# Kernel optimization log

Measured on AMD Instinct MI355X. Metric: run time of the kernel, lower is better.

Reference implementation:

```python
import jax, jax.numpy as jnp
import numpy as np

B, D, L, H = 8, 512, 2048, 8
DH = D // H
NEG = -1e30


def setup_inputs() -> dict:
    key = jax.random.key(0)
    k1, k2, k3, k4 = jax.random.split(key, 4)
    queries = jax.random.normal(k1, (B, D, L), dtype=jnp.float32)
    mask = jax.random.randint(k2, (B, L), 0, 2, dtype=jnp.int32)
    w_mem = jax.random.normal(k3, (2 * D, D), dtype=jnp.float32) * (1.0 / np.sqrt(D))
    w_q = jax.random.normal(k4, (D, D), dtype=jnp.float32) * (1.0 / np.sqrt(D))
    return {"queries": queries, "mask": mask, "w_mem": w_mem, "w_q": w_q}


def reference(queries, mask, w_mem, w_q):
    # 1x1 conv == pointwise GEMM over channel dim. queries: [B, D, L]
    memory = jnp.einsum('od,bdl->blo', w_mem, queries)  # [B, L, 2D]
    query = jnp.einsum('od,bdl->blo', w_q, queries)     # [B, L, D]

    def split_heads(x):  # [B, L, C] -> [B, H, L, C/H]
        b, l, c = x.shape
        return x.reshape(b, l, H, c // H).transpose(0, 2, 1, 3)

    k, v = memory[..., :D], memory[..., D:]
    Q = split_heads(query) * (DH ** -0.5)  # [B, H, L, DH]
    K = split_heads(k)
    V = split_heads(v)

    logits = jnp.einsum('bhqd,bhkd->bhqk', Q, K)  # [B, H, L, L]
    m = mask.astype(jnp.float32)[:, None, None, :]  # [B, 1, 1, L]
    logits = logits * m + (1.0 - m) * NEG
    weights = jax.nn.softmax(logits, axis=-1)
    x = jnp.einsum('bhqk,bhkd->bhqd', weights, V)  # [B, H, L, DH]
    # combine heads -> [B, L, D] -> transpose back to [B, D, L]
    out = x.transpose(0, 2, 1, 3).reshape(B, L, D).transpose(0, 2, 1)
    return out
```

## Files before the change

### kernel.cpp

```cpp
#include <hip/hip_runtime.h>
#include <hip/hip_bf16.h>

#define NB 8
#define ND 512
#define NL 2048
#define NH 8
#define NDH 64
#define VROWS 72

typedef __attribute__((ext_vector_type(8))) short bf16x8;
typedef __attribute__((ext_vector_type(4))) float f32x4;
typedef __attribute__((ext_vector_type(4))) unsigned int u32x4;

__device__ __forceinline__ unsigned short f2bf(float x) {
    return (unsigned short)((__float_as_uint(x) + 0x8000u) >> 16);
}

__device__ __forceinline__ float exp2_fast(float x) {
#if __has_builtin(__builtin_amdgcn_exp2f)
    return __builtin_amdgcn_exp2f(x);
#else
    return exp2f(x);
#endif
}

__device__ __forceinline__ unsigned int pack_bf16(float a, float b) {
#if __has_builtin(__builtin_amdgcn_cvt_pk_bf16_f32)
    auto r = __builtin_amdgcn_cvt_pk_bf16_f32(a, b);
    unsigned int u;
    __builtin_memcpy(&u, &r, 4);
    return u;
#else
    unsigned int ua = __float_as_uint(a) + 0x8000u;
    unsigned int ub = __float_as_uint(b) + 0x8000u;
    return __builtin_amdgcn_perm(ub, ua, 0x07060302u);
#endif
}

__device__ __forceinline__ void async16(void* lds, const void* g) {
    __builtin_amdgcn_global_load_lds(
        (const __attribute__((address_space(1))) unsigned int*)g,
        (__attribute__((address_space(3))) unsigned int*)lds, 16, 0, 0);
}

__global__ __launch_bounds__(256) void prep(
    const float* __restrict__ qin,
    const float* __restrict__ w_mem, const float* __restrict__ w_q,
    const int* __restrict__ maskp,
    unsigned short* __restrict__ Xt, unsigned short* __restrict__ Wc,
    unsigned short* __restrict__ Vt)
{
    const int bid = blockIdx.x;
    const int t = threadIdx.x;
    if (bid < 2048) {
        __shared__ __align__(16) unsigned short T[64][72];
        const int l0 = (bid & 31) * 64, d0 = ((bid >> 5) & 7) * 64, b = bid >> 8;
        const float* X = qin + ((size_t)b * ND + d0) * NL + l0;
        #pragma unroll
        for (int i = 0; i < 4; ++i) {
            int e = t + i * 256;
            int d = e >> 4, l4 = (e & 15) * 4;
            float4 v = *(const float4*)(X + (size_t)d * NL + l4);
            T[l4 + 0][d] = f2bf(v.x);
            T[l4 + 1][d] = f2bf(v.y);
            T[l4 + 2][d] = f2bf(v.z);
            T[l4 + 3][d] = f2bf(v.w);
        }
        __syncthreads();
        #pragma unroll
        for (int i = 0; i < 2; ++i) {
            int e = t + i * 256;
            int row = e >> 3, c8 = (e & 7) * 8;
            *(bf16x8*)(Xt + ((size_t)b * NL + l0 + row) * ND + d0 + c8) =
                *(const bf16x8*)&T[row][c8];
        }
    } else if (bid < 2432) {
        int idx = ((bid - 2048) * 256 + t) * 8;
        int o = idx >> 9, k = idx & 511;
        const float* src;
        float sc;
        if (o < 1024) { src = w_mem + (size_t)o * ND + k; sc = 1.0f; }
        else          { src = w_q + (size_t)(o - 1024) * ND + k;
                        sc = 0.125f * 1.4426950408889634f; }
        float4 f0 = *(const float4*)src;
        float4 f1 = *(const float4*)(src + 4);
        ushort4 p0 = { f2bf(f0.x * sc), f2bf(f0.y * sc), f2bf(f0.z * sc), f2bf(f0.w * sc) };
        ushort4 p1 = { f2bf(f1.x * sc), f2bf(f1.y * sc), f2bf(f1.z * sc), f2bf(f1.w * sc) };
        *(ushort4*)(Wc + idx) = p0;
        *(ushort4*)(Wc + idx + 4) = p1;
    } else {
        const int bh = bid - 2432;
        const int b = bh >> 3;
        unsigned short* row64 = Vt + ((size_t)bh * VROWS + 64) * NL;
        for (int kk = t; kk < NL; kk += 256) {
            int s = (kk & 32) | ((kk & 12) << 1) | ((kk & 16) >> 2) | (kk & 3);
            row64[(kk & ~63) | s] =
                maskp[b * NL + kk] ? (unsigned short)0x3F80 : (unsigned short)0;
        }
    }
}

__global__ __launch_bounds__(256, 3) void proj_mfma(
    const unsigned short* __restrict__ Wc,
    const unsigned short* __restrict__ Xt,
    const int* __restrict__ maskp,
    unsigned short* __restrict__ Kh,
    unsigned short* __restrict__ Qh,
    unsigned short* __restrict__ Vt)
{
    __shared__ __align__(16) unsigned short As[128 * 64];
    __shared__ __align__(16) unsigned short Bs[128 * 64];

    const int b  = blockIdx.z;
    const int m0 = blockIdx.y * 128;
    const int n0 = blockIdx.x * 128;
    const int t  = threadIdx.x;
    const int w = t >> 6, lane = t & 63, quad = lane >> 4, lq = lane & 15;
    const int wo = (w >> 1) * 64, wl = (w & 1) * 64;
    const int lr = lane >> 3;
    const int cbsw = (lane & 7) ^ lr;
    const bool isV = (m0 >= 512) && (m0 < 1024);
    const f32x4 z4 = {0.f, 0.f, 0.f, 0.f};
    const int sw[2] = {(quad ^ (lq & 7)) * 8, ((4 + quad) ^ (lq & 7)) * 8};

    f32x4 acc[4][4];
    #pragma unroll
    for (int im = 0; im < 4; ++im)
        #pragma unroll
        for (int in = 0; in < 4; ++in) acc[im][in] = z4;

    if (!isV) {
        for (int k0 = 0; k0 < ND; k0 += 64) {
            __syncthreads();
            #pragma unroll 2
            for (int i = w; i < 32; i += 4) {
                if (i < 16) {
                    int R = i * 8;
                    async16(&As[R * 64],
                            Wc + (size_t)(m0 + R + lr) * ND + k0 + cbsw * 8);
                } else {
                    int R = (i - 16) * 8;
                    async16(&Bs[R * 64],
                            Xt + ((size_t)b * NL + n0 + R + lr) * ND + k0 + cbsw * 8);
                }
            }
            __syncthreads();
            #pragma unroll
            for (int ks = 0; ks < 2; ++ks) {
                bf16x8 af[4], bfr[4];
                #pragma unroll
                for (int im = 0; im < 4; ++im)
                    af[im] = *(const bf16x8*)&As[(wo + im * 16 + lq) * 64 + sw[ks]];
                #pragma unroll
                for (int in = 0; in < 4; ++in)
                    bfr[in] = *(const bf16x8*)&Bs[(wl + in * 16 + lq) * 64 + sw[ks]];
                #pragma unroll
                for (int im = 0; im < 4; ++im)
                    #pragma unroll
                    for (int in = 0; in < 4; ++in)
                        acc[im][in] = __builtin_amdgcn_mfma_f32_16x16x32_bf16(
                            af[im], bfr[in], acc[im][in], 0, 0, 0);
            }
        }
        unsigned short* dst = (m0 < 512) ? Kh : Qh;
        #pragma unroll
        for (int im = 0; im < 4; ++im) {
            int o  = (m0 + wo + im * 16 + quad * 4) & 511;
            int hh = o >> 6, dh = o & 63;
            #pragma unroll
            for (int in = 0; in < 4; ++in) {
                int l = n0 + wl + in * 16 + lq;
                ushort4 pk = { f2bf(acc[im][in][0]), f2bf(acc[im][in][1]),
                               f2bf(acc[im][in][2]), f2bf(acc[im][in][3]) };
                *(ushort4*)&dst[(((size_t)b * NH + hh) * NL + l) * NDH + dh] = pk;
            }
        }
    } else {
        for (int k0 = 0; k0 < ND; k0 += 64) {
            __syncthreads();
            #pragma unroll 2
            for (int i = w; i < 32; i += 4) {
                if (i < 16) {
                    int R = i * 8;
                    async16(&As[R * 64],
                            Wc + (size_t)(m0 + R + lr) * ND + k0 + cbsw * 8);
                } else {
                    int R = (i - 16) * 8;
                    async16(&Bs[R * 64],
                            Xt + ((size_t)b * NL + n0 + R + lr) * ND + k0 + cbsw * 8);
                }
            }
            __syncthreads();
            #pragma unroll
            for (int ks = 0; ks < 2; ++ks) {
                bf16x8 af[4], bfr[4];
                #pragma unroll
                for (int im = 0; im < 4; ++im)
                    af[im] = *(const bf16x8*)&As[(wo + im * 16 + lq) * 64 + sw[ks]];
                #pragma unroll
                for (int in = 0; in < 4; ++in)
                    bfr[in] = *(const bf16x8*)&Bs[(wl + in * 16 + lq) * 64 + sw[ks]];
                #pragma unroll
                for (int im = 0; im < 4; ++im)
                    #pragma unroll
                    for (int in = 0; in < 4; ++in)
                        acc[im][in] = __builtin_amdgcn_mfma_f32_16x16x32_bf16(
                            bfr[im], af[in], acc[im][in], 0, 0, 0);
            }
        }
        #pragma unroll
        for (int im = 0; im < 4; ++im) {
            int l4 = n0 + wl + im * 16 + quad * 4;
            int kk = l4 & 63;
            int s4 = (kk & 32) | ((kk & 12) << 1) | ((kk & 16) >> 2);
            int lp = (l4 & ~63) | s4;
            int4 m4 = *(const int4*)&maskp[b * NL + l4];
            float mv[4] = {(float)m4.x, (float)m4.y, (float)m4.z, (float)m4.w};
            #pragma unroll
            for (int in = 0; in < 4; ++in) {
                int o  = m0 - 512 + wo + in * 16 + lq;
                int hh = o >> 6, dd = o & 63;
                ushort4 pk = { f2bf(acc[im][in][0] * mv[0]),
                               f2bf(acc[im][in][1] * mv[1]),
                               f2bf(acc[im][in][2] * mv[2]),
                               f2bf(acc[im][in][3] * mv[3]) };
                *(ushort4*)&Vt[(((size_t)(b * NH + hh)) * VROWS + dd) * NL + lp] = pk;
            }
        }
    }
}

__global__ __launch_bounds__(512, 4) void attn_mfma(
    const unsigned short* __restrict__ Qh,
    const unsigned short* __restrict__ Kh,
    const unsigned short* __restrict__ Vt,
    float* __restrict__ out)
{
    __shared__ __align__(16) unsigned short Ks2[2][64 * 64];
    __shared__ __align__(16) unsigned short Vs2[2][80 * 64];

    const int id = blockIdx.x;
    const int h  = id & 7;
    const int b  = (id >> 3) & 7;
    const int q0 = (id >> 6) * 256;
    const int t = threadIdx.x;
    const int w = t >> 6;
    const int lane = t & 63, quad = lane >> 4, lq = lane & 15;
    const int lr = lane >> 3;
    const int cbsw = (lane & 7) ^ lr;
    const f32x4 z4 = {0.f, 0.f, 0.f, 0.f};

    const unsigned short* Qg = Qh + ((size_t)(b * NH + h)) * NL * NDH;
    const unsigned short* Kg = Kh + ((size_t)(b * NH + h)) * NL * NDH;
    const unsigned short* Vg = Vt + ((size_t)(b * NH + h)) * VROWS * NL;

    const int sw0 = (quad ^ (lq & 7)) * 8;
    const int sw1 = ((4 + quad) ^ (lq & 7)) * 8;

    const unsigned short* kgp = Kg + (size_t)(w * 8 + lr) * NDH + cbsw * 8;
    const unsigned short* vgp = Vg + (size_t)(w * 8 + lr) * NL + cbsw * 8;
    const unsigned short* vgm = Vg + (size_t)(64 + lr) * NL + cbsw * 8;

    auto stage = [&](unsigned short* Kd, unsigned short* Vd, int kn) {
        async16(Kd + w * 512, kgp + (size_t)kn * NDH);
        async16(Vd + w * 512, vgp + kn);
        if (w == 7) async16(Vd + 8 * 512, vgm + kn);
    };

    stage(Ks2[0], Vs2[0], 0);

    bf16x8 qf[2][2];
    #pragma unroll
    for (int ni = 0; ni < 2; ++ni)
        #pragma unroll
        for (int ks = 0; ks < 2; ++ks)
            qf[ni][ks] = *(const bf16x8*)
                &Qg[(size_t)(q0 + w * 32 + ni * 16 + lq) * NDH + ks * 32 + quad * 8];

    f32x4 oacc[5][2];
    #pragma unroll
    for (int dm = 0; dm < 5; ++dm)
        #pragma unroll
        for (int ni = 0; ni < 2; ++ni) oacc[dm][ni] = z4;

    auto body = [&](const unsigned short* KsB, const unsigned short* VsB,
                    unsigned short* KsN, unsigned short* VsN,
                    int kn, bool pf) {
        __syncthreads();
        if (pf) stage(KsN, VsN, kn);

        const unsigned short* kb0 = KsB + lq * 64 + sw0;
        const unsigned short* kb1 = KsB + lq * 64 + sw1;
        const unsigned short* vb0 = VsB + lq * 64 + sw0;
        const unsigned short* vb1 = VsB + lq * 64 + sw1;

        f32x4 sacc[4][2];
        #pragma unroll
        for (int mi = 0; mi < 4; ++mi) {
            bf16x8 kf = *(const bf16x8*)&kb0[mi * 1024];
            sacc[mi][0] = __builtin_amdgcn_mfma_f32_16x16x32_bf16(kf, qf[0][0], z4, 0, 0, 0);
            sacc[mi][1] = __builtin_amdgcn_mfma_f32_16x16x32_bf16(kf, qf[1][0], z4, 0, 0, 0);
        }
        #pragma unroll
        for (int mi = 0; mi < 4; ++mi) {
            bf16x8 kf = *(const bf16x8*)&kb1[mi * 1024];
            sacc[mi][0] = __builtin_amdgcn_mfma_f32_16x16x32_bf16(kf, qf[0][1], sacc[mi][0], 0, 0, 0);
            sacc[mi][1] = __builtin_amdgcn_mfma_f32_16x16x32_bf16(kf, qf[1][1], sacc[mi][1], 0, 0, 0);
        }

        #pragma unroll
        for (int ks = 0; ks < 2; ++ks) {
            u32x4 pfu[2];
            #pragma unroll
            for (int half = 0; half < 2; ++half) {
                const int mi = ks * 2 + half, jp = half * 2;
                #pragma unroll
                for (int ni = 0; ni < 2; ++ni) {
                    float e0 = exp2_fast(sacc[mi][ni][0]);
                    float e1 = exp2_fast(sacc[mi][ni][1]);
                    float e2 = exp2_fast(sacc[mi][ni][2]);
                    float e3 = exp2_fast(sacc[mi][ni][3]);
                    pfu[ni][jp + 0] = pack_bf16(e0, e1);
                    pfu[ni][jp + 1] = pack_bf16(e2, e3);
                }
            }
            const unsigned short* vb = ks ? vb1 : vb0;
            #pragma unroll
            for (int dm = 0; dm < 5; ++dm) {
                bf16x8 vf = *(const bf16x8*)&vb[dm * 1024];
                oacc[dm][0] = __builtin_amdgcn_mfma_f32_16x16x32_bf16(
                    vf, __builtin_bit_cast(bf16x8, pfu[0]), oacc[dm][0], 0, 0, 0);
                oacc[dm][1] = __builtin_amdgcn_mfma_f32_16x16x32_bf16(
                    vf, __builtin_bit_cast(bf16x8, pfu[1]), oacc[dm][1], 0, 0, 0);
            }
        }
    };

    for (int k0 = 0; k0 < NL; k0 += 128) {
        body(Ks2[0], Vs2[0], Ks2[1], Vs2[1], k0 + 64, true);
        body(Ks2[1], Vs2[1], Ks2[0], Vs2[0], k0 + 128, k0 + 128 < NL);
    }

    float inv[2];
    #pragma unroll
    for (int ni = 0; ni < 2; ++ni)
        inv[ni] = 1.0f / __shfl(oacc[4][ni][0], lq);

    #pragma unroll
    for (int dm = 0; dm < 4; ++dm)
        #pragma unroll
        for (int ni = 0; ni < 2; ++ni)
            #pragma unroll
            for (int r = 0; r < 4; ++r) {
                int dh = dm * 16 + quad * 4 + r;
                int l  = q0 + w * 32 + ni * 16 + lq;
                out[((size_t)b * ND + h * NDH + dh) * NL + l] =
                    oacc[dm][ni][r] * inv[ni];
            }
}

extern "C" void kernel_launch(void* const* d_in, const int* in_sizes, int n_in,
                              void* d_out, int out_size, void* d_ws, size_t ws_size,
                              hipStream_t stream) {
    const float* queries = (const float*)d_in[0];
    const int*   maskp   = (const int*)d_in[1];
    const float* w_mem   = (const float*)d_in[2];
    const float* w_q     = (const float*)d_in[3];
    float* out = (float*)d_out;

    const size_t headElems  = (size_t)NB * NH * NL * NDH;
    const size_t vElems     = (size_t)NB * NH * VROWS * NL;
    unsigned short* Kh = (unsigned short*)d_ws;
    unsigned short* Vt = Kh + headElems;
    unsigned short* Qh = Vt + vElems;
    unsigned short* Wc = Qh + headElems;
    unsigned short* Xt = Wc + (size_t)1536 * ND;

    prep<<<2496, 256, 0, stream>>>(queries, w_mem, w_q, maskp, Xt, Wc, Vt);

    dim3 g1(NL / 128, 1536 / 128, NB);
    proj_mfma<<<g1, 256, 0, stream>>>(Wc, Xt, maskp, Kh, Qh, Vt);

    attn_mfma<<<512, 512, 0, stream>>>(Qh, Kh, Vt, out);
}
```

Measured before the change: 190.3 us.

## Double-buffer projection GEMM and software-pipeline QK with softmax/PV in attention

The projection kernel now double-buffers its A and B shared-memory tiles, so the next k-slice loads while the current one is multiplied. Occupancy is lowered to 2 blocks to fit the extra LDS. The attention kernel moves to a 4-deep K/V ring buffer and a software pipeline: QK scores for the next tile are computed while exp and PV run on the current tile's scores. This aims to hide global-load latency and interleave MFMA with transcendental work, at the cost of more LDS and registers, which may reduce occupancy.

```diff
diff --git a/kernel.cpp b/kernel.cpp
--- a/kernel.cpp
+++ b/kernel.cpp
@@ -100,7 +100,7 @@
     }
 }
 
-__global__ __launch_bounds__(256, 3) void proj_mfma(
+__global__ __launch_bounds__(256, 2) void proj_mfma(
     const unsigned short* __restrict__ Wc,
     const unsigned short* __restrict__ Xt,
     const int* __restrict__ maskp,
@@ -108,8 +108,8 @@
     unsigned short* __restrict__ Qh,
     unsigned short* __restrict__ Vt)
 {
-    __shared__ __align__(16) unsigned short As[128 * 64];
-    __shared__ __align__(16) unsigned short Bs[128 * 64];
+    __shared__ __align__(16) unsigned short As[2][128 * 64];
+    __shared__ __align__(16) unsigned short Bs[2][128 * 64];
 
     const int b  = blockIdx.z;
     const int m0 = blockIdx.y * 128;
@@ -123,37 +123,44 @@
     const f32x4 z4 = {0.f, 0.f, 0.f, 0.f};
     const int sw[2] = {(quad ^ (lq & 7)) * 8, ((4 + quad) ^ (lq & 7)) * 8};
 
+    auto stageP = [&](int bi, int k0) {
+        #pragma unroll 2
+        for (int i = w; i < 32; i += 4) {
+            if (i < 16) {
+                int R = i * 8;
+                async16(&As[bi][R * 64],
+                        Wc + (size_t)(m0 + R + lr) * ND + k0 + cbsw * 8);
+            } else {
+                int R = (i - 16) * 8;
+                async16(&Bs[bi][R * 64],
+                        Xt + ((size_t)b * NL + n0 + R + lr) * ND + k0 + cbsw * 8);
+            }
+        }
+    };
+
     f32x4 acc[4][4];
     #pragma unroll
     for (int im = 0; im < 4; ++im)
         #pragma unroll
         for (int in = 0; in < 4; ++in) acc[im][in] = z4;
 
+    stageP(0, 0);
+
     if (!isV) {
+        #pragma unroll 2
         for (int k0 = 0; k0 < ND; k0 += 64) {
+            const int bi = (k0 >> 6) & 1;
             __syncthreads();
-            #pragma unroll 2
-            for (int i = w; i < 32; i += 4) {
-                if (i < 16) {
-                    int R = i * 8;
-                    async16(&As[R * 64],
-                            Wc + (size_t)(m0 + R + lr) * ND + k0 + cbsw * 8);
-                } else {
-                    int R = (i - 16) * 8;
-                    async16(&Bs[R * 64],
-                            Xt + ((size_t)b * NL + n0 + R + lr) * ND + k0 + cbsw * 8);
-                }
-            }
-            __syncthreads();
+            if (k0 + 64 < ND) stageP(bi ^ 1, k0 + 64);
             #pragma unroll
             for (int ks = 0; ks < 2; ++ks) {
                 bf16x8 af[4], bfr[4];
                 #pragma unroll
                 for (int im = 0; im < 4; ++im)
-                    af[im] = *(const bf16x8*)&As[(wo + im * 16 + lq) * 64 + sw[ks]];
+                    af[im] = *(const bf16x8*)&As[bi][(wo + im * 16 + lq) * 64 + sw[ks]];
                 #pragma unroll
                 for (int in = 0; in < 4; ++in)
-                    bfr[in] = *(const bf16x8*)&Bs[(wl + in * 16 + lq) * 64 + sw[ks]];
+                    bfr[in] = *(const bf16x8*)&Bs[bi][(wl + in * 16 + lq) * 64 + sw[ks]];
                 #pragma unroll
                 for (int im = 0; im < 4; ++im)
                     #pragma unroll
@@ -176,30 +183,20 @@
             }
         }
     } else {
+        #pragma unroll 2
         for (int k0 = 0; k0 < ND; k0 += 64) {
+            const int bi = (k0 >> 6) & 1;
             __syncthreads();
-            #pragma unroll 2
-            for (int i = w; i < 32; i += 4) {
-                if (i < 16) {
-                    int R = i * 8;
-                    async16(&As[R * 64],
-                            Wc + (size_t)(m0 + R + lr) * ND + k0 + cbsw * 8);
-                } else {
-                    int R = (i - 16) * 8;
-                    async16(&Bs[R * 64],
-                            Xt + ((size_t)b * NL + n0 + R + lr) * ND + k0 + cbsw * 8);
-                }
-            }
-            __syncthreads();
+            if (k0 + 64 < ND) stageP(bi ^ 1, k0 + 64);
             #pragma unroll
             for (int ks = 0; ks < 2; ++ks) {
                 bf16x8 af[4], bfr[4];
                 #pragma unroll
                 for (int im = 0; im < 4; ++im)
-                    af[im] = *(const bf16x8*)&As[(wo + im * 16 + lq) * 64 + sw[ks]];
+                    af[im] = *(const bf16x8*)&As[bi][(wo + im * 16 + lq) * 64 + sw[ks]];
                 #pragma unroll
                 for (int in = 0; in < 4; ++in)
-                    bfr[in] = *(const bf16x8*)&Bs[(wl + in * 16 + lq) * 64 + sw[ks]];
+                    bfr[in] = *(const bf16x8*)&Bs[bi][(wl + in * 16 + lq) * 64 + sw[ks]];
                 #pragma unroll
                 for (int im = 0; im < 4; ++im)
                     #pragma unroll
@@ -236,8 +233,8 @@
     const unsigned short* __restrict__ Vt,
     float* __restrict__ out)
 {
-    __shared__ __align__(16) unsigned short Ks2[2][64 * 64];
-    __shared__ __align__(16) unsigned short Vs2[2][80 * 64];
+    __shared__ __align__(16) unsigned short Ks4[4][64 * 64];
+    __shared__ __align__(16) unsigned short Vs4[4][80 * 64];
 
     const int id = blockIdx.x;
     const int h  = id & 7;
@@ -261,13 +258,13 @@
     const unsigned short* vgp = Vg + (size_t)(w * 8 + lr) * NL + cbsw * 8;
     const unsigned short* vgm = Vg + (size_t)(64 + lr) * NL + cbsw * 8;
 
-    auto stage = [&](unsigned short* Kd, unsigned short* Vd, int kn) {
-        async16(Kd + w * 512, kgp + (size_t)kn * NDH);
-        async16(Vd + w * 512, vgp + kn);
-        if (w == 7) async16(Vd + 8 * 512, vgm + kn);
+    auto stage = [&](int bi, int kn) {
+        async16(&Ks4[bi][w * 512], kgp + (size_t)kn * NDH);
+        async16(&Vs4[bi][w * 512], vgp + kn);
+        if (w == 7) async16(&Vs4[bi][8 * 512], vgm + kn);
     };
 
-    stage(Ks2[0], Vs2[0], 0);
+    stage(0, 0);
 
     bf16x8 qf[2][2];
     #pragma unroll
@@ -283,63 +280,86 @@
         #pragma unroll
         for (int ni = 0; ni < 2; ++ni) oacc[dm][ni] = z4;
 
-    auto body = [&](const unsigned short* KsB, const unsigned short* VsB,
-                    unsigned short* KsN, unsigned short* VsN,
-                    int kn, bool pf) {
+    f32x4 sA[4][2], sB[4][2];
+
+    __syncthreads();
+    stage(1, 64);
+
+    #pragma unroll
+    for (int mi = 0; mi < 4; ++mi) {
+        bf16x8 kf0 = *(const bf16x8*)&Ks4[0][(mi * 16 + lq) * 64 + sw0];
+        bf16x8 kf1 = *(const bf16x8*)&Ks4[0][(mi * 16 + lq) * 64 + sw1];
+        #pragma unroll
+        for (int ni = 0; ni < 2; ++ni) {
+            f32x4 s = __builtin_amdgcn_mfma_f32_16x16x32_bf16(kf0, qf[ni][0], z4, 0, 0, 0);
+            sA[mi][ni] = __builtin_amdgcn_mfma_f32_16x16x32_bf16(kf1, qf[ni][1], s, 0, 0, 0);
+        }
+    }
+
+    auto body = [&](int cur, int nxt, int fre, int kn2,
+                    f32x4 (&SIN)[4][2], f32x4 (&SOUT)[4][2],
+                    bool dostage, bool doqk) {
         __syncthreads();
-        if (pf) stage(KsN, VsN, kn);
-
-        const unsigned short* kb0 = KsB + lq * 64 + sw0;
-        const unsigned short* kb1 = KsB + lq * 64 + sw1;
-        const unsigned short* vb0 = VsB + lq * 64 + sw0;
-        const unsigned short* vb1 = VsB + lq * 64 + sw1;
-
-        f32x4 sacc[4][2];
+        if (dostage) stage(fre, kn2);
+        u32x4 p0[2], p1[2];
         #pragma unroll
         for (int mi = 0; mi < 4; ++mi) {
-            bf16x8 kf = *(const bf16x8*)&kb0[mi * 1024];
-            sacc[mi][0] = __builtin_amdgcn_mfma_f32_16x16x32_bf16(kf, qf[0][0], z4, 0, 0, 0);
-            sacc[mi][1] = __builtin_amdgcn_mfma_f32_16x16x32_bf16(kf, qf[1][0], z4, 0, 0, 0);
-        }
-        #pragma unroll
-        for (int mi = 0; mi < 4; ++mi) {
-            bf16x8 kf = *(const bf16x8*)&kb1[mi * 1024];
-            sacc[mi][0] = __builtin_amdgcn_mfma_f32_16x16x32_bf16(kf, qf[0][1], sacc[mi][0], 0, 0, 0);
-            sacc[mi][1] = __builtin_amdgcn_mfma_f32_16x16x32_bf16(kf, qf[1][1], sacc[mi][1], 0, 0, 0);
-        }
-
-        #pragma unroll
-        for (int ks = 0; ks < 2; ++ks) {
-            u32x4 pfu[2];
-            #pragma unroll
-            for (int half = 0; half < 2; ++half) {
-                const int mi = ks * 2 + half, jp = half * 2;
+            if (doqk) {
+                bf16x8 kf0 = *(const bf16x8*)&Ks4[nxt][(mi * 16 + lq) * 64 + sw0];
+                bf16x8 kf1 = *(const bf16x8*)&Ks4[nxt][(mi * 16 + lq) * 64 + sw1];
                 #pragma unroll
                 for (int ni = 0; ni < 2; ++ni) {
-                    float e0 = exp2_fast(sacc[mi][ni][0]);
-                    float e1 = exp2_fast(sacc[mi][ni][1]);
-                    float e2 = exp2_fast(sacc[mi][ni][2]);
-                    float e3 = exp2_fast(sacc[mi][ni][3]);
-                    pfu[ni][jp + 0] = pack_bf16(e0, e1);
-                    pfu[ni][jp + 1] = pack_bf16(e2, e3);
+                    f32x4 s = __builtin_amdgcn_mfma_f32_16x16x32_bf16(kf0, qf[ni][0], z4, 0, 0, 0);
+                    SOUT[mi][ni] = __builtin_amdgcn_mfma_f32_16x16x32_bf16(kf1, qf[ni][1], s, 0, 0, 0);
                 }
             }
-            const unsigned short* vb = ks ? vb1 : vb0;
-            #pragma unroll
-            for (int dm = 0; dm < 5; ++dm) {
-                bf16x8 vf = *(const bf16x8*)&vb[dm * 1024];
-                oacc[dm][0] = __builtin_amdgcn_mfma_f32_16x16x32_bf16(
-                    vf, __builtin_bit_cast(bf16x8, pfu[0]), oacc[dm][0], 0, 0, 0);
-                oacc[dm][1] = __builtin_amdgcn_mfma_f32_16x16x32_bf16(
-                    vf, __builtin_bit_cast(bf16x8, pfu[1]), oacc[dm][1], 0, 0, 0);
+            const int jp = (mi & 1) * 2;
+            #pragma unroll
+            for (int ni = 0; ni < 2; ++ni) {
+                float e0 = exp2_fast(SIN[mi][ni][0]);
+                float e1 = exp2_fast(SIN[mi][ni][1]);
+                float e2 = exp2_fast(SIN[mi][ni][2]);
+                float e3 = exp2_fast(SIN[mi][ni][3]);
+                unsigned int d0 = pack_bf16(e0, e1);
+                unsigned int d1 = pack_bf16(e2, e3);
+                if (mi < 2) { p0[ni][jp] = d0; p0[ni][jp + 1] = d1; }
+                else        { p1[ni][jp] = d0; p1[ni][jp + 1] = d1; }
+            }
+            if (mi == 1) {
+                #pragma unroll
+                for (int dm = 0; dm < 5; ++dm) {
+                    bf16x8 vf = *(const bf16x8*)&Vs4[cur][(dm * 16 + lq) * 64 + sw0];
+                    oacc[dm][0] = __builtin_amdgcn_mfma_f32_16x16x32_bf16(
+                        vf, __builtin_bit_cast(bf16x8, p0[0]), oacc[dm][0], 0, 0, 0);
+                    oacc[dm][1] = __builtin_amdgcn_mfma_f32_16x16x32_bf16(
+                        vf, __builtin_bit_cast(bf16x8, p0[1]), oacc[dm][1], 0, 0, 0);
+                }
+            }
+            if (mi == 3) {
+                #pragma unroll
+                for (int dm = 0; dm < 5; ++dm) {
+                    bf16x8 vf = *(const bf16x8*)&Vs4[cur][(dm * 16 + lq) * 64 + sw1];
+                    oacc[dm][0] = __builtin_amdgcn_mfma_f32_16x16x32_bf16(
+                        vf, __builtin_bit_cast(bf16x8, p1[0]), oacc[dm][0], 0, 0, 0);
+                    oacc[dm][1] = __builtin_amdgcn_mfma_f32_16x16x32_bf16(
+                        vf, __builtin_bit_cast(bf16x8, p1[1]), oacc[dm][1], 0, 0, 0);
+                }
             }
         }
     };
 
-    for (int k0 = 0; k0 < NL; k0 += 128) {
-        body(Ks2[0], Vs2[0], Ks2[1], Vs2[1], k0 + 64, true);
-        body(Ks2[1], Vs2[1], Ks2[0], Vs2[0], k0 + 128, k0 + 128 < NL);
+    #pragma unroll 1
+    for (int t4 = 0; t4 < 28; t4 += 4) {
+        const int k = t4 * 64;
+        body(0, 1, 2, k + 128, sA, sB, true, true);
+        body(1, 2, 3, k + 192, sB, sA, true, true);
+        body(2, 3, 0, k + 256, sA, sB, true, true);
+        body(3, 0, 1, k + 320, sB, sA, true, true);
     }
+    body(0, 1, 2, 30 * 64, sA, sB, true, true);
+    body(1, 2, 3, 31 * 64, sB, sA, true, true);
+    body(2, 3, 0, 0,       sA, sB, false, true);
+    body(3, 0, 1, 0,       sB, sA, false, false);
 
     float inv[2];
     #pragma unroll
```

Result: slower. 238.6 us (+25.3%).

## Compact unmasked keys/values so attention iterates only over valid key tiles

Applied to the files above, without the earlier changes.

The prep kernel computes a per-batch prefix sum over the key mask, producing a compaction map and a count of 64-key tiles. The projection scatters K and V rows only for unmasked positions into compacted slots, and zero-fills the padding of the last tile. The attention loop then runs over just the valid tiles instead of all 2048 keys, roughly halving QK and PV work for a random mask. It adds scattered, scalar V stores and a dependency on the mask being sparse.

```diff
diff --git a/kernel.cpp b/kernel.cpp
--- a/kernel.cpp
+++ b/kernel.cpp
@@ -37,6 +37,10 @@
 #endif
 }
 
+__device__ __forceinline__ int perm64(int k) {
+    return (k & 32) | ((k & 12) << 1) | ((k & 16) >> 2) | (k & 3);
+}
+
 __device__ __forceinline__ void async16(void* lds, const void* g) {
     __builtin_amdgcn_global_load_lds(
         (const __attribute__((address_space(1))) unsigned int*)g,
@@ -48,7 +52,8 @@
     const float* __restrict__ w_mem, const float* __restrict__ w_q,
     const int* __restrict__ maskp,
     unsigned short* __restrict__ Xt, unsigned short* __restrict__ Wc,
-    unsigned short* __restrict__ Vt)
+    unsigned short* __restrict__ Vt, unsigned short* __restrict__ Kh,
+    int* __restrict__ cmap, int* __restrict__ ntile)
 {
     const int bid = blockIdx.x;
     const int t = threadIdx.x;
@@ -89,13 +94,47 @@
         *(ushort4*)(Wc + idx) = p0;
         *(ushort4*)(Wc + idx + 4) = p1;
     } else {
-        const int bh = bid - 2432;
-        const int b = bh >> 3;
-        unsigned short* row64 = Vt + ((size_t)bh * VROWS + 64) * NL;
-        for (int kk = t; kk < NL; kk += 256) {
-            int s = (kk & 32) | ((kk & 12) << 1) | ((kk & 16) >> 2) | (kk & 3);
-            row64[(kk & ~63) | s] =
-                maskp[b * NL + kk] ? (unsigned short)0x3F80 : (unsigned short)0;
+        __shared__ int wsum[4];
+        const int b = bid - 2432;
+        const int lane = t & 63, wv = t >> 6;
+        int4 ma = *(const int4*)&maskp[b * NL + t * 8];
+        int4 mb = *(const int4*)&maskp[b * NL + t * 8 + 4];
+        int m[8] = {ma.x, ma.y, ma.z, ma.w, mb.x, mb.y, mb.z, mb.w};
+        int loc = 0;
+        #pragma unroll
+        for (int i = 0; i < 8; ++i) loc += m[i];
+        int sc = loc;
+        #pragma unroll
+        for (int off = 1; off < 64; off <<= 1) {
+            int v = __shfl_up(sc, off);
+            if (lane >= off) sc += v;
+        }
+        if (lane == 63) wsum[wv] = sc;
+        __syncthreads();
+        int wbase = 0;
+        #pragma unroll
+        for (int i = 0; i < 4; ++i) if (i < wv) wbase += wsum[i];
+        int j = wbase + sc - loc;
+        #pragma unroll
+        for (int i = 0; i < 8; ++i) {
+            cmap[b * NL + t * 8 + i] = m[i] ? j : -1;
+            j += m[i];
+        }
+        const int nb = wsum[0] + wsum[1] + wsum[2] + wsum[3];
+        const int Nt = (nb + 63) & ~63;
+        if (t == 0) ntile[b] = Nt >> 6;
+        const int pad = Nt - nb;
+        for (int h = 0; h < NH; ++h) {
+            unsigned short* row64 = Vt + (((size_t)(b * NH + h)) * VROWS + 64) * NL;
+            for (int jj = t; jj < Nt; jj += 256)
+                row64[(jj & ~63) | perm64(jj & 63)] =
+                    (jj < nb) ? (unsigned short)0x3F80 : (unsigned short)0;
+            for (int e = t; e < pad * 64; e += 256) {
+                int jj = nb + (e >> 6), dd = e & 63;
+                int slot = (jj & ~63) | perm64(jj & 63);
+                Vt[(((size_t)(b * NH + h)) * VROWS + dd) * NL + slot] = 0;
+                Kh[(((size_t)(b * NH + h)) * NL + jj) * NDH + dd] = 0;
+            }
         }
     }
 }
@@ -103,7 +142,7 @@
 __global__ __launch_bounds__(256, 3) void proj_mfma(
     const unsigned short* __restrict__ Wc,
     const unsigned short* __restrict__ Xt,
-    const int* __restrict__ maskp,
+    const int* __restrict__ cmap,
     unsigned short* __restrict__ Kh,
     unsigned short* __restrict__ Qh,
     unsigned short* __restrict__ Vt)
@@ -162,17 +201,36 @@
                             af[im], bfr[in], acc[im][in], 0, 0, 0);
             }
         }
-        unsigned short* dst = (m0 < 512) ? Kh : Qh;
-        #pragma unroll
-        for (int im = 0; im < 4; ++im) {
-            int o  = (m0 + wo + im * 16 + quad * 4) & 511;
-            int hh = o >> 6, dh = o & 63;
-            #pragma unroll
-            for (int in = 0; in < 4; ++in) {
-                int l = n0 + wl + in * 16 + lq;
-                ushort4 pk = { f2bf(acc[im][in][0]), f2bf(acc[im][in][1]),
-                               f2bf(acc[im][in][2]), f2bf(acc[im][in][3]) };
-                *(ushort4*)&dst[(((size_t)b * NH + hh) * NL + l) * NDH + dh] = pk;
+        if (m0 < 512) {
+            int j[4];
+            #pragma unroll
+            for (int in = 0; in < 4; ++in)
+                j[in] = cmap[b * NL + n0 + wl + in * 16 + lq];
+            #pragma unroll
+            for (int im = 0; im < 4; ++im) {
+                int o  = (m0 + wo + im * 16 + quad * 4) & 511;
+                int hh = o >> 6, dh = o & 63;
+                #pragma unroll
+                for (int in = 0; in < 4; ++in) {
+                    if (j[in] >= 0) {
+                        ushort4 pk = { f2bf(acc[im][in][0]), f2bf(acc[im][in][1]),
+                                       f2bf(acc[im][in][2]), f2bf(acc[im][in][3]) };
+                        *(ushort4*)&Kh[(((size_t)b * NH + hh) * NL + j[in]) * NDH + dh] = pk;
+                    }
+                }
+            }
+        } else {
+            #pragma unroll
+            for (int im = 0; im < 4; ++im) {
+                int o  = (m0 + wo + im * 16 + quad * 4) & 511;
+                int hh = o >> 6, dh = o & 63;
+                #pragma unroll
+                for (int in = 0; in < 4; ++in) {
+                    int l = n0 + wl + in * 16 + lq;
+                    ushort4 pk = { f2bf(acc[im][in][0]), f2bf(acc[im][in][1]),
+                                   f2bf(acc[im][in][2]), f2bf(acc[im][in][3]) };
+                    *(ushort4*)&Qh[(((size_t)b * NH + hh) * NL + l) * NDH + dh] = pk;
+                }
             }
         }
     } else {
@@ -211,20 +269,21 @@
         #pragma unroll
         for (int im = 0; im < 4; ++im) {
             int l4 = n0 + wl + im * 16 + quad * 4;
-            int kk = l4 & 63;
-            int s4 = (kk & 32) | ((kk & 12) << 1) | ((kk & 16) >> 2);
-            int lp = (l4 & ~63) | s4;
-            int4 m4 = *(const int4*)&maskp[b * NL + l4];
-            float mv[4] = {(float)m4.x, (float)m4.y, (float)m4.z, (float)m4.w};
+            int4 j4 = *(const int4*)&cmap[b * NL + l4];
+            int jj[4] = {j4.x, j4.y, j4.z, j4.w};
+            int slot[4];
+            #pragma unroll
+            for (int r = 0; r < 4; ++r)
+                slot[r] = (jj[r] & ~63) | perm64(jj[r] & 63);
             #pragma unroll
             for (int in = 0; in < 4; ++in) {
                 int o  = m0 - 512 + wo + in * 16 + lq;
                 int hh = o >> 6, dd = o & 63;
-                ushort4 pk = { f2bf(acc[im][in][0] * mv[0]),
-                               f2bf(acc[im][in][1] * mv[1]),
-                               f2bf(acc[im][in][2] * mv[2]),
-                               f2bf(acc[im][in][3] * mv[3]) };
-                *(ushort4*)&Vt[(((size_t)(b * NH + hh)) * VROWS + dd) * NL + lp] = pk;
+                const size_t rowbase = (((size_t)(b * NH + hh)) * VROWS + dd) * NL;
+                #pragma unroll
+                for (int r = 0; r < 4; ++r)
+                    if (jj[r] >= 0)
+                        Vt[rowbase + slot[r]] = f2bf(acc[im][in][r]);
             }
         }
     }
@@ -234,6 +293,7 @@
     const unsigned short* __restrict__ Qh,
     const unsigned short* __restrict__ Kh,
     const unsigned short* __restrict__ Vt,
+    const int* __restrict__ ntilep,
     float* __restrict__ out)
 {
     __shared__ __align__(16) unsigned short Ks2[2][64 * 64];
@@ -253,6 +313,7 @@
     const unsigned short* Qg = Qh + ((size_t)(b * NH + h)) * NL * NDH;
     const unsigned short* Kg = Kh + ((size_t)(b * NH + h)) * NL * NDH;
     const unsigned short* Vg = Vt + ((size_t)(b * NH + h)) * VROWS * NL;
+    const int ntiles = ntilep[b];
 
     const int sw0 = (quad ^ (lq & 7)) * 8;
     const int sw1 = ((4 + quad) ^ (lq & 7)) * 8;
@@ -336,10 +397,14 @@
         }
     };
 
-    for (int k0 = 0; k0 < NL; k0 += 128) {
-        body(Ks2[0], Vs2[0], Ks2[1], Vs2[1], k0 + 64, true);
-        body(Ks2[1], Vs2[1], Ks2[0], Vs2[0], k0 + 128, k0 + 128 < NL);
+    int kt = 0;
+    #pragma unroll 1
+    for (; kt + 2 <= ntiles; kt += 2) {
+        body(Ks2[0], Vs2[0], Ks2[1], Vs2[1], (kt + 1) * 64, true);
+        body(Ks2[1], Vs2[1], Ks2[0], Vs2[0], (kt + 2) * 64, kt + 2 < ntiles);
     }
+    if (kt < ntiles)
+        body(Ks2[0], Vs2[0], Ks2[1], Vs2[1], 0, false);
 
     float inv[2];
     #pragma unroll
@@ -375,11 +440,14 @@
     unsigned short* Qh = Vt + vElems;
     unsigned short* Wc = Qh + headElems;
     unsigned short* Xt = Wc + (size_t)1536 * ND;
-
-    prep<<<2496, 256, 0, stream>>>(queries, w_mem, w_q, maskp, Xt, Wc, Vt);
+    int* cmap  = (int*)(Xt + (size_t)NB * NL * ND);
+    int* ntile = cmap + NB * NL;
+
+    prep<<<2440, 256, 0, stream>>>(queries, w_mem, w_q, maskp,
+                                   Xt, Wc, Vt, Kh, cmap, ntile);
 
     dim3 g1(NL / 128, 1536 / 128, NB);
-    proj_mfma<<<g1, 256, 0, stream>>>(Wc, Xt, maskp, Kh, Qh, Vt);
-
-    attn_mfma<<<512, 512, 0, stream>>>(Qh, Kh, Vt, out);
-}
+    proj_mfma<<<g1, 256, 0, stream>>>(Wc, Xt, cmap, Kh, Qh, Vt);
+
+    attn_mfma<<<512, 512, 0, stream>>>(Qh, Kh, Vt, ntile, out);
+}
```

New measurement: 184.2 us. -3.2%, faster.
